# Optimization experiments

Hardware: AMD Instinct MI355X
Metric: run time of the kernel (lower is better)

The kernel has to match this reference:

```python
import jax, jax.numpy as jnp
import numpy as np

TOK_DIM = 512
POS_DIM = 512
N_HEADS = 16
HEAD_DIM = 64
D_MODEL = 1024
INNER = N_HEADS * HEAD_DIM
B, T = 4, 2048


def setup_inputs() -> dict:
    key = jax.random.key(0)
    ks = jax.random.split(key, 5)
    s = 0.02
    return {
        "x": jax.random.normal(ks[0], (B, T, TOK_DIM + POS_DIM), dtype=jnp.float32),
        "Wq": jax.random.normal(ks[1], (POS_DIM, INNER), dtype=jnp.float32) * s,
        "Wk": jax.random.normal(ks[2], (POS_DIM, INNER), dtype=jnp.float32) * s,
        "Wv": jax.random.normal(ks[3], (TOK_DIM, INNER), dtype=jnp.float32) * s,
        "Wo": jax.random.normal(ks[4], (INNER, D_MODEL), dtype=jnp.float32) * s,
    }


def reference(x, Wq, Wk, Wv, Wo):
    b, t, _ = x.shape
    x_tok = x[:, :, :TOK_DIM]
    x_pos = x[:, :, TOK_DIM:]
    # project and split heads: [B, H, T, Dh]
    q = (x_pos @ Wq).reshape(b, t, N_HEADS, HEAD_DIM).transpose(0, 2, 1, 3)
    k = (x_pos @ Wk).reshape(b, t, N_HEADS, HEAD_DIM).transpose(0, 2, 1, 3)
    v = (x_tok @ Wv).reshape(b, t, N_HEADS, HEAD_DIM).transpose(0, 2, 1, 3)
    att = jnp.einsum("bhqd,bhkd->bhqk", q, k) / jnp.sqrt(jnp.float32(HEAD_DIM))
    causal = jnp.tril(jnp.ones((t, t), dtype=bool))
    att = jnp.where(causal, att, -jnp.inf)
    att = jax.nn.softmax(att, axis=-1)
    out = jnp.einsum("bhqk,bhkd->bhqd", att, v)
    out = out.transpose(0, 2, 1, 3).reshape(b, t, INNER)
    return out @ Wo
```

## Files before the change

### kernel.cpp

```cpp
#include <hip/hip_runtime.h>
#include <stdint.h>


typedef unsigned short u16;
typedef __bf16 bf16;
typedef bf16 bf16x8 __attribute__((ext_vector_type(8)));
typedef u16 u16x8 __attribute__((ext_vector_type(8)));
typedef u16 u16x4 __attribute__((ext_vector_type(4)));
typedef float f32x4 __attribute__((ext_vector_type(4)));
typedef uint32_t u32x4 __attribute__((ext_vector_type(4)));

__device__ __forceinline__ u16 cvt_bf16(float f) {
  uint32_t u = __builtin_bit_cast(uint32_t, f);
  u += 0x7FFFu + ((u >> 16) & 1u);
  return (u16)(u >> 16);
}

__device__ __forceinline__ uint32_t pack2_bf16(float lo, float hi) {
  uint32_t a = __builtin_bit_cast(uint32_t, lo) + 0x8000u;
  uint32_t b = __builtin_bit_cast(uint32_t, hi) + 0x8000u;
  return __builtin_amdgcn_perm(b, a, 0x07060302u);
}

__device__ __forceinline__ f32x4 mfma_bf(bf16x8 a, bf16x8 b, f32x4 c) {
  return __builtin_amdgcn_mfma_f32_16x16x32_bf16(a, b, c, 0, 0, 0);
}

typedef __attribute__((address_space(1))) const uint32_t g_u32;
typedef __attribute__((address_space(3))) uint32_t l_u32;
__device__ __forceinline__ void gload16(const u16* g, u16* l) {
  __builtin_amdgcn_global_load_lds((g_u32*)g, (l_u32*)l, 16, 0, 0);
}

__global__ __launch_bounds__(256) void prep_x(
    const float* __restrict__ x, u16* __restrict__ xtok,
    u16* __restrict__ xpos) {
  int idx = blockIdx.x * 256 + threadIdx.x;
  int row = idx >> 8;
  int c4 = (idx & 255) * 4;
  float4 v = *(const float4*)(x + (size_t)row * 1024 + c4);
  u16x4 b = {cvt_bf16(v.x), cvt_bf16(v.y), cvt_bf16(v.z), cvt_bf16(v.w)};
  u16* dst = (c4 < 512) ? (xtok + (size_t)row * 512 + c4)
                        : (xpos + (size_t)row * 512 + c4 - 512);
  *(u16x4*)dst = b;
}

__global__ __launch_bounds__(256) void prep_w(
    const float* __restrict__ Wq, const float* __restrict__ Wk,
    const float* __restrict__ Wv, const float* __restrict__ Wo,
    u16* __restrict__ Wt, u16* __restrict__ WoT) {
  const int z = blockIdx.z;
  const float* src = (z == 0) ? Wq : (z == 1) ? Wk : (z == 2) ? Wv : Wo;
  const int K = (z == 3) ? 1024 : 512;
  u16* dst = (z == 3) ? WoT : (Wt + (size_t)z * 1024 * 512);
  const int k0 = blockIdx.y * 64, n0 = blockIdx.x * 64;
  if (k0 >= K) return;
  __shared__ u16 T[64][68];
  const int tid = threadIdx.x;
  const int r = tid >> 4, c = (tid & 15) * 4;
#pragma unroll
  for (int i = 0; i < 4; i++) {
    float4 v = *(const float4*)(src + (size_t)(k0 + r + i * 16) * 1024 + n0 + c);
    u16x4 b = {cvt_bf16(v.x), cvt_bf16(v.y), cvt_bf16(v.z), cvt_bf16(v.w)};
    *(u16x4*)&T[r + i * 16][c] = b;
  }
  __syncthreads();
#pragma unroll
  for (int i = 0; i < 4; i++) {
    int n = r + i * 16;
    u16x4 v;
#pragma unroll
    for (int j = 0; j < 4; j++) v[j] = T[c + j][n];
    *(u16x4*)(dst + (size_t)(n0 + n) * K + k0 + c) = v;
  }
}

__global__ __launch_bounds__(256) void gemm_qkv(
    const u16* __restrict__ xtok, const u16* __restrict__ xpos,
    const u16* __restrict__ Wt, u16* __restrict__ qkv) {
  const int z = blockIdx.z;
  const u16* A = (z == 2) ? xtok : xpos;
  const u16* Bt = Wt + (size_t)z * 1024 * 512;
  u16* outp = qkv + (size_t)z * (64u * 2048u * 64u);
  const float osc = (z == 0) ? 0.18033688011112042f : 1.0f;

  const int m0 = blockIdx.y * 128;
  const int n0 = blockIdx.x * 128;
  const int tid = threadIdx.x;
  const int lane = tid & 63;
  const int w = tid >> 6;
  const int wm = (w & 1) * 64;
  const int wn = (w >> 1) * 64;
  const int mrow = lane & 15;
  const int quad = lane >> 4;

  __shared__ __align__(16) u16 Ash[128 * 32];
  __shared__ __align__(16) u16 Bsh[128 * 32];

  f32x4 acc[4][4];
#pragma unroll
  for (int i = 0; i < 4; i++)
#pragma unroll
    for (int j = 0; j < 4; j++) acc[i][j] = (f32x4){0.f, 0.f, 0.f, 0.f};

  const int sr = w * 16 + (lane >> 2);
  const int sc = (lane & 3) * 8;
  const u16* gA = A + (size_t)(m0 + sr) * 512 + sc;
  const u16* gB = Bt + (size_t)(n0 + sr) * 512 + sc;
  u16* lA = Ash + sr * 32 + sc;
  u16* lB = Bsh + sr * 32 + sc;

  for (int kb = 0; kb < 512; kb += 32) {
    __syncthreads();
    gload16(gA + kb, lA);
    gload16(gA + 64 * 512 + kb, lA + 64 * 32);
    gload16(gB + kb, lB);
    gload16(gB + 64 * 512 + kb, lB + 64 * 32);
    __syncthreads();

    bf16x8 af[4], bfr[4];
#pragma unroll
    for (int mi = 0; mi < 4; mi++)
      af[mi] = *(const bf16x8*)(Ash + (wm + mi * 16 + mrow) * 32 + quad * 8);
#pragma unroll
    for (int ni = 0; ni < 4; ni++)
      bfr[ni] = *(const bf16x8*)(Bsh + (wn + ni * 16 + mrow) * 32 + quad * 8);
#pragma unroll
    for (int mi = 0; mi < 4; mi++)
#pragma unroll
      for (int ni = 0; ni < 4; ni++)
        acc[mi][ni] = mfma_bf(af[mi], bfr[ni], acc[mi][ni]);
  }

#pragma unroll
  for (int mi = 0; mi < 4; mi++)
#pragma unroll
    for (int ni = 0; ni < 4; ni++)
#pragma unroll
      for (int r = 0; r < 4; r++) {
        int m = m0 + wm + mi * 16 + quad * 4 + r;
        int n = n0 + wn + ni * 16 + mrow;
        int bb = m >> 11, t = m & 2047;
        int h = n >> 6, d = n & 63;
        outp[(((size_t)(bb * 16 + h)) * 2048 + t) * 64 + d] =
            cvt_bf16(acc[mi][ni][r] * osc);
      }
}

__global__ __launch_bounds__(256) void vtrans(
    const u16* __restrict__ vnat, u16* __restrict__ vperm) {
  const int bh = blockIdx.y;
  const int t0 = blockIdx.x * 64;
  const u16* src = vnat + (size_t)bh * (2048 * 64);
  u16* dst = vperm + (size_t)bh * (64 * 2048);
  __shared__ __align__(16) u16 Tsh[64][72];
  const int tid = threadIdx.x;
#pragma unroll
  for (int i = 0; i < 2; i++) {
    int r = (tid >> 3) + 32 * i;
    int c = (tid & 7) * 8;
    *(u16x8*)&Tsh[r][c] = *(const u16x8*)(src + (size_t)(t0 + r) * 64 + c);
  }
  __syncthreads();
  const int d = tid >> 2;
  const int q = tid & 3;
  u16* drow = dst + (size_t)d * 2048 + t0 + (q >> 1) * 32 + (q & 1) * 4;
#pragma unroll
  for (int a = 0; a < 4; a++) {
    u16x4 v;
#pragma unroll
    for (int b = 0; b < 4; b++) v[b] = Tsh[q * 16 + a * 4 + b][d];
    *(u16x4*)(drow + a * 8) = v;
  }
}

__global__ __launch_bounds__(256, 4) void attn(
    const u16* __restrict__ qkv, const u16* __restrict__ vperm,
    u16* __restrict__ aout) {
  const int bh = blockIdx.x;
  const int sp = blockIdx.y;
  const int bb = bh >> 4, h = bh & 15;
  const u16* Qp = qkv + (size_t)bh * (2048 * 64);
  const u16* Kp = qkv + (size_t)(64 + bh) * (2048 * 64);
  const u16* Vp = vperm + (size_t)bh * (64 * 2048);

  __shared__ __align__(16) u16 Ksh0[64 * 32], Ksh1[64 * 32];
  __shared__ __align__(16) u16 Vsh0[64 * 32], Vsh1[64 * 32];
  __shared__ __align__(16) u16 Osh[4][16][72];

  const int tid = threadIdx.x;
  const int lane = tid & 63;
  const int w = tid >> 6;
  const int mrow = lane & 15;
  const int quad = lane >> 4;
  const int srow = w * 16 + (lane >> 2);
  const int sc = (lane & 3) * 8;

  const u16x8 onesu = {0x3F80, 0x3F80, 0x3F80, 0x3F80,
                       0x3F80, 0x3F80, 0x3F80, 0x3F80};
  const bf16x8 ones = __builtin_bit_cast(bf16x8, onesu);

  for (int half = 0; half < 2; ++half) {
    const int qt = (half == 0) ? sp : 31 - sp;
    const int q0 = qt * 64;
    const int nk = qt + 1;

    const u16* qrow = Qp + (size_t)(q0 + w * 16 + mrow) * 64 + quad * 8;
    const bf16x8 qf0 = *(const bf16x8*)qrow;
    const bf16x8 qf1 = *(const bf16x8*)(qrow + 32);
    f32x4 o[4], ol;
#pragma unroll
    for (int dt = 0; dt < 4; ++dt) o[dt] = (f32x4){0.f, 0.f, 0.f, 0.f};
    ol = (f32x4){0.f, 0.f, 0.f, 0.f};

    for (int it = 0; it < nk; ++it) {
      const int k0 = it * 64;
      __syncthreads();
      {
        const u16* kg = Kp + (size_t)(k0 + srow) * 64 + sc;
        u16x8 a0 = *(const u16x8*)kg;
        u16x8 a1 = *(const u16x8*)(kg + 32);
        const u16* vg = Vp + (size_t)srow * 2048 + k0 + sc;
        u16x8 b0 = *(const u16x8*)vg;
        u16x8 b1 = *(const u16x8*)(vg + 32);
        *(u16x8*)(Ksh0 + srow * 32 + sc) = a0;
        *(u16x8*)(Ksh1 + srow * 32 + sc) = a1;
        *(u16x8*)(Vsh0 + srow * 32 + sc) = b0;
        *(u16x8*)(Vsh1 + srow * 32 + sc) = b1;
      }
      __syncthreads();

      f32x4 s[4];
#pragma unroll
      for (int nt = 0; nt < 4; ++nt) {
        bf16x8 kf0 = *(const bf16x8*)(Ksh0 + (nt * 16 + mrow) * 32 + quad * 8);
        bf16x8 kf1 = *(const bf16x8*)(Ksh1 + (nt * 16 + mrow) * 32 + quad * 8);
        f32x4 zz = (f32x4){0.f, 0.f, 0.f, 0.f};
        zz = mfma_bf(kf0, qf0, zz);
        zz = mfma_bf(kf1, qf1, zz);
        s[nt] = zz;
      }

      if (it == nk - 1) {
        const int q = q0 + w * 16 + mrow;
#pragma unroll
        for (int nt = 0; nt < 4; ++nt)
#pragma unroll
          for (int r = 0; r < 4; ++r)
            if (k0 + nt * 16 + quad * 4 + r > q) s[nt][r] = -1e30f;
      }
#pragma unroll
      for (int nt = 0; nt < 4; ++nt)
#pragma unroll
        for (int r = 0; r < 4; ++r)
          s[nt][r] = __builtin_amdgcn_exp2f(s[nt][r]);

      u32x4 w0 = {pack2_bf16(s[0][0], s[0][1]), pack2_bf16(s[0][2], s[0][3]),
                  pack2_bf16(s[1][0], s[1][1]), pack2_bf16(s[1][2], s[1][3])};
      u32x4 w1 = {pack2_bf16(s[2][0], s[2][1]), pack2_bf16(s[2][2], s[2][3]),
                  pack2_bf16(s[3][0], s[3][1]), pack2_bf16(s[3][2], s[3][3])};
      bf16x8 pf0 = __builtin_bit_cast(bf16x8, w0);
      bf16x8 pf1 = __builtin_bit_cast(bf16x8, w1);

      ol = mfma_bf(ones, pf0, ol);
      ol = mfma_bf(ones, pf1, ol);
#pragma unroll
      for (int dt = 0; dt < 4; ++dt) {
        bf16x8 vf0 = *(const bf16x8*)(Vsh0 + (dt * 16 + mrow) * 32 + quad * 8);
        bf16x8 vf1 = *(const bf16x8*)(Vsh1 + (dt * 16 + mrow) * 32 + quad * 8);
        o[dt] = mfma_bf(vf0, pf0, o[dt]);
        o[dt] = mfma_bf(vf1, pf1, o[dt]);
      }
    }

    const float inv = 1.f / ol[0];
#pragma unroll
    for (int dt = 0; dt < 4; ++dt)
#pragma unroll
      for (int r = 0; r < 4; ++r)
        Osh[w][mrow][dt * 16 + quad * 4 + r] = cvt_bf16(o[dt][r] * inv);
#pragma unroll
    for (int p = 0; p < 2; ++p) {
      int ql = (lane >> 3) + 8 * p;
      int ch = lane & 7;
      u16x8 v = *(const u16x8*)&Osh[w][ql][ch * 8];
      int t = q0 + w * 16 + ql;
      *(u16x8*)(aout + ((size_t)(bb * 2048 + t)) * 1024 + h * 64 + ch * 8) = v;
    }
  }
}

__global__ __launch_bounds__(256) void gemm_out(
    const u16* __restrict__ Am, const u16* __restrict__ WoT,
    float* __restrict__ out) {
  const int m0 = blockIdx.y * 128;
  const int n0 = blockIdx.x * 128;
  const int tid = threadIdx.x;
  const int lane = tid & 63;
  const int w = tid >> 6;
  const int wm = (w & 1) * 64;
  const int wn = (w >> 1) * 64;
  const int mrow = lane & 15;
  const int quad = lane >> 4;

  __shared__ __align__(16) u16 Ash[128 * 32];
  __shared__ __align__(16) u16 Bsh[128 * 32];

  f32x4 acc[4][4];
#pragma unroll
  for (int i = 0; i < 4; i++)
#pragma unroll
    for (int j = 0; j < 4; j++) acc[i][j] = (f32x4){0.f, 0.f, 0.f, 0.f};

  const int sr = w * 16 + (lane >> 2);
  const int sc = (lane & 3) * 8;
  const u16* gA = Am + (size_t)(m0 + sr) * 1024 + sc;
  const u16* gB = WoT + (size_t)(n0 + sr) * 1024 + sc;
  u16* lA = Ash + sr * 32 + sc;
  u16* lB = Bsh + sr * 32 + sc;

  for (int kb = 0; kb < 1024; kb += 32) {
    __syncthreads();
    gload16(gA + kb, lA);
    gload16(gA + 64 * 1024 + kb, lA + 64 * 32);
    gload16(gB + kb, lB);
    gload16(gB + 64 * 1024 + kb, lB + 64 * 32);
    __syncthreads();

    bf16x8 af[4], bfr[4];
#pragma unroll
    for (int mi = 0; mi < 4; mi++)
      af[mi] = *(const bf16x8*)(Ash + (wm + mi * 16 + mrow) * 32 + quad * 8);
#pragma unroll
    for (int ni = 0; ni < 4; ni++)
      bfr[ni] = *(const bf16x8*)(Bsh + (wn + ni * 16 + mrow) * 32 + quad * 8);
#pragma unroll
    for (int mi = 0; mi < 4; mi++)
#pragma unroll
      for (int ni = 0; ni < 4; ni++)
        acc[mi][ni] = mfma_bf(af[mi], bfr[ni], acc[mi][ni]);
  }

#pragma unroll
  for (int mi = 0; mi < 4; mi++)
#pragma unroll
    for (int ni = 0; ni < 4; ni++)
#pragma unroll
      for (int r = 0; r < 4; r++) {
        int m = m0 + wm + mi * 16 + quad * 4 + r;
        int n = n0 + wn + ni * 16 + mrow;
        out[(size_t)m * 1024 + n] = acc[mi][ni][r];
      }
}

extern "C" void kernel_launch(void* const* d_in, const int* in_sizes, int n_in,
                              void* d_out, int out_size, void* d_ws, size_t ws_size,
                              hipStream_t stream) {
  const float* x  = (const float*)d_in[0];
  const float* Wq = (const float*)d_in[1];
  const float* Wk = (const float*)d_in[2];
  const float* Wv = (const float*)d_in[3];
  const float* Wo = (const float*)d_in[4];

  u16* qkv   = (u16*)d_ws;
  u16* vperm = qkv + (size_t)3 * 64 * 2048 * 64;
  u16* aout  = vperm + (size_t)64 * 64 * 2048;
  u16* xtok  = aout + (size_t)8192 * 1024;
  u16* xpos  = xtok + (size_t)8192 * 512;
  u16* Wt    = xpos + (size_t)8192 * 512;
  u16* WoT   = Wt + (size_t)3 * 1024 * 512;
  float* out = (float*)d_out;

  prep_x<<<dim3(8192), dim3(256), 0, stream>>>(x, xtok, xpos);
  prep_w<<<dim3(16, 16, 4), dim3(256), 0, stream>>>(Wq, Wk, Wv, Wo, Wt, WoT);
  gemm_qkv<<<dim3(8, 64, 3), dim3(256), 0, stream>>>(xtok, xpos, Wt, qkv);
  vtrans<<<dim3(32, 64), dim3(256), 0, stream>>>(
      qkv + (size_t)2 * 64 * 2048 * 64, vperm);
  attn<<<dim3(64, 16), dim3(256), 0, stream>>>(qkv, vperm, aout);
  gemm_out<<<dim3(8, 64), dim3(256), 0, stream>>>(aout, WoT, out);
}
```

Before: 229.2 us.

## Fuse V transpose into QKV GEMM epilogue and prefetch K/V tiles in attention

The QKV GEMM now writes V directly in the permuted, transposed layout that attention consumes, which removes the separate vtrans kernel launch and its extra read/write pass over V. The attention loop also loads the next K/V tile into registers while the current tile is being computed, a software-prefetch pipeline meant to hide global load latency. The V epilogue writes with a 2048-element stride per element, which may produce poorly coalesced stores. The register prefetch adds register pressure under launch bounds that target 4 blocks.

```diff
diff --git a/kernel.cpp b/kernel.cpp
--- a/kernel.cpp
+++ b/kernel.cpp
@@ -77,7 +77,8 @@
 
 __global__ __launch_bounds__(256) void gemm_qkv(
     const u16* __restrict__ xtok, const u16* __restrict__ xpos,
-    const u16* __restrict__ Wt, u16* __restrict__ qkv) {
+    const u16* __restrict__ Wt, u16* __restrict__ qkv,
+    u16* __restrict__ vperm) {
   const int z = blockIdx.z;
   const u16* A = (z == 2) ? xtok : xpos;
   const u16* Bt = Wt + (size_t)z * 1024 * 512;
@@ -132,45 +133,37 @@
         acc[mi][ni] = mfma_bf(af[mi], bfr[ni], acc[mi][ni]);
   }
 
-#pragma unroll
-  for (int mi = 0; mi < 4; mi++)
-#pragma unroll
-    for (int ni = 0; ni < 4; ni++)
-#pragma unroll
-      for (int r = 0; r < 4; r++) {
-        int m = m0 + wm + mi * 16 + quad * 4 + r;
-        int n = n0 + wn + ni * 16 + mrow;
-        int bb = m >> 11, t = m & 2047;
-        int h = n >> 6, d = n & 63;
-        outp[(((size_t)(bb * 16 + h)) * 2048 + t) * 64 + d] =
-            cvt_bf16(acc[mi][ni][r] * osc);
-      }
-}
-
-__global__ __launch_bounds__(256) void vtrans(
-    const u16* __restrict__ vnat, u16* __restrict__ vperm) {
-  const int bh = blockIdx.y;
-  const int t0 = blockIdx.x * 64;
-  const u16* src = vnat + (size_t)bh * (2048 * 64);
-  u16* dst = vperm + (size_t)bh * (64 * 2048);
-  __shared__ __align__(16) u16 Tsh[64][72];
-  const int tid = threadIdx.x;
-#pragma unroll
-  for (int i = 0; i < 2; i++) {
-    int r = (tid >> 3) + 32 * i;
-    int c = (tid & 7) * 8;
-    *(u16x8*)&Tsh[r][c] = *(const u16x8*)(src + (size_t)(t0 + r) * 64 + c);
-  }
-  __syncthreads();
-  const int d = tid >> 2;
-  const int q = tid & 3;
-  u16* drow = dst + (size_t)d * 2048 + t0 + (q >> 1) * 32 + (q & 1) * 4;
-#pragma unroll
-  for (int a = 0; a < 4; a++) {
-    u16x4 v;
-#pragma unroll
-    for (int b = 0; b < 4; b++) v[b] = Tsh[q * 16 + a * 4 + b][d];
-    *(u16x4*)(drow + a * 8) = v;
+  if (z != 2) {
+#pragma unroll
+    for (int mi = 0; mi < 4; mi++)
+#pragma unroll
+      for (int ni = 0; ni < 4; ni++)
+#pragma unroll
+        for (int r = 0; r < 4; r++) {
+          int m = m0 + wm + mi * 16 + quad * 4 + r;
+          int n = n0 + wn + ni * 16 + mrow;
+          int bb = m >> 11, t = m & 2047;
+          int h = n >> 6, d = n & 63;
+          outp[(((size_t)(bb * 16 + h)) * 2048 + t) * 64 + d] =
+              cvt_bf16(acc[mi][ni][r] * osc);
+        }
+  } else {
+#pragma unroll
+    for (int mi = 0; mi < 4; mi++)
+#pragma unroll
+      for (int ni = 0; ni < 4; ni++)
+#pragma unroll
+        for (int r = 0; r < 4; r++) {
+          int m = m0 + wm + mi * 16 + quad * 4 + r;
+          int n = n0 + wn + ni * 16 + mrow;
+          int bb = m >> 11, t = m & 2047;
+          int h = n >> 6, d = n & 63;
+          int k6 = t & 63;
+          int pos = (k6 & 32) + ((k6 >> 4) & 1) * 4 + ((k6 >> 2) & 3) * 8 +
+                    (k6 & 3);
+          vperm[(((size_t)(bb * 16 + h)) * 64 + d) * 2048 + (t & ~63) + pos] =
+              cvt_bf16(acc[mi][ni][r]);
+        }
   }
 }
 
@@ -200,6 +193,9 @@
                        0x3F80, 0x3F80, 0x3F80, 0x3F80};
   const bf16x8 ones = __builtin_bit_cast(bf16x8, onesu);
 
+  const u16* kgb = Kp + (size_t)srow * 64 + sc;
+  const u16* vgb = Vp + (size_t)srow * 2048 + sc;
+
   for (int half = 0; half < 2; ++half) {
     const int qt = (half == 0) ? sp : 31 - sp;
     const int q0 = qt * 64;
@@ -213,23 +209,28 @@
     for (int dt = 0; dt < 4; ++dt) o[dt] = (f32x4){0.f, 0.f, 0.f, 0.f};
     ol = (f32x4){0.f, 0.f, 0.f, 0.f};
 
+    u16x8 ka0 = *(const u16x8*)kgb;
+    u16x8 ka1 = *(const u16x8*)(kgb + 32);
+    u16x8 va0 = *(const u16x8*)vgb;
+    u16x8 va1 = *(const u16x8*)(vgb + 32);
+
     for (int it = 0; it < nk; ++it) {
+      __syncthreads();
+      *(u16x8*)(Ksh0 + srow * 32 + sc) = ka0;
+      *(u16x8*)(Ksh1 + srow * 32 + sc) = ka1;
+      *(u16x8*)(Vsh0 + srow * 32 + sc) = va0;
+      *(u16x8*)(Vsh1 + srow * 32 + sc) = va1;
+      __syncthreads();
+
+      if (it + 1 < nk) {
+        const int kn = (it + 1) * 64;
+        ka0 = *(const u16x8*)(kgb + (size_t)kn * 64);
+        ka1 = *(const u16x8*)(kgb + (size_t)kn * 64 + 32);
+        va0 = *(const u16x8*)(vgb + kn);
+        va1 = *(const u16x8*)(vgb + kn + 32);
+      }
+
       const int k0 = it * 64;
-      __syncthreads();
-      {
-        const u16* kg = Kp + (size_t)(k0 + srow) * 64 + sc;
-        u16x8 a0 = *(const u16x8*)kg;
-        u16x8 a1 = *(const u16x8*)(kg + 32);
-        const u16* vg = Vp + (size_t)srow * 2048 + k0 + sc;
-        u16x8 b0 = *(const u16x8*)vg;
-        u16x8 b1 = *(const u16x8*)(vg + 32);
-        *(u16x8*)(Ksh0 + srow * 32 + sc) = a0;
-        *(u16x8*)(Ksh1 + srow * 32 + sc) = a1;
-        *(u16x8*)(Vsh0 + srow * 32 + sc) = b0;
-        *(u16x8*)(Vsh1 + srow * 32 + sc) = b1;
-      }
-      __syncthreads();
-
       f32x4 s[4];
 #pragma unroll
       for (int nt = 0; nt < 4; ++nt) {
@@ -373,9 +374,7 @@
 
   prep_x<<<dim3(8192), dim3(256), 0, stream>>>(x, xtok, xpos);
   prep_w<<<dim3(16, 16, 4), dim3(256), 0, stream>>>(Wq, Wk, Wv, Wo, Wt, WoT);
-  gemm_qkv<<<dim3(8, 64, 3), dim3(256), 0, stream>>>(xtok, xpos, Wt, qkv);
-  vtrans<<<dim3(32, 64), dim3(256), 0, stream>>>(
-      qkv + (size_t)2 * 64 * 2048 * 64, vperm);
+  gemm_qkv<<<dim3(8, 64, 3), dim3(256), 0, stream>>>(xtok, xpos, Wt, qkv, vperm);
   attn<<<dim3(64, 16), dim3(256), 0, stream>>>(qkv, vperm, aout);
   gemm_out<<<dim3(8, 64), dim3(256), 0, stream>>>(aout, WoT, out);
 }
```

New measurement: 223.6 us. 2.4% less time.
